# Kernel optimization log

Hardware: AMD Instinct MI355X
Metric: run time of the kernel (lower is better)

Reference implementation:

```python
import jax, jax.numpy as jnp
import numpy as np

LMAX = 4
NC = (LMAX + 1) ** 2          # 25 spherical coefficients
L0 = LMAX + 1                 # number of m=0 coefficients
SPHERE = 128
CIN1 = 2 * SPHERE             # concat(source, target) channels
HID = 64
HEADS = 8
ALPHA_C = 64
VAL_C = 16
OUT_C = 128
GRID = 2 * (LMAX + 1)         # S2 grid resolution
N_NODES = 2500
N_EDGES = 25000
MAX_ELEM = 90
EDGE_IN = 128 + 2 * 64        # distance basis + src/tgt atom embeddings
M_SIZES = [LMAX - m + 1 for m in range(1, LMAX + 1)]  # l-count per |m|>0
RAD_OUT = L0 * CIN1 + sum(s * CIN1 for s in M_SIZES)  # 3840

def _lm(l, m):
    return l * l + l + m
_p = [_lm(l, 0) for l in range(LMAX + 1)]
for m in range(1, LMAX + 1):
    _p += [_lm(l, -m) for l in range(m, LMAX + 1)]
    _p += [_lm(l, m) for l in range(m, LMAX + 1)]
PERM = np.asarray(_p)             # l-primary -> m-primary
INV_PERM = np.argsort(PERM)       # m-primary -> l-primary
EXPAND = np.concatenate([np.full(2 * l + 1, l) for l in range(LMAX + 1)])

def _layernorm(x, g, b, eps=1e-5):
    mu = jnp.mean(x, axis=-1, keepdims=True)
    var = jnp.mean((x - mu) ** 2, axis=-1, keepdims=True)
    return (x - mu) * jax.lax.rsqrt(var + eps) * g + b

def _so2_conv(xm, fc0_w, fc0_b, wms, cin, mout, extra, rad):
    # xm: [E, NC, cin] in m-primary layout. Per-order SO(2) 'complex' conv.
    E = xm.shape[0]
    x0 = xm[:, :L0].reshape(E, L0 * cin)
    off_rad = L0 * cin
    if rad is not None:
        x0 = x0 * rad[:, :off_rad]
    x0 = x0 @ fc0_w + fc0_b
    x0_extra = None
    if extra:
        x0_extra = x0[:, :extra]
        x0 = x0[:, extra:]
    outs = [x0.reshape(E, L0, mout)]
    off = L0
    for i, sz in enumerate(M_SIZES):
        xb = xm[:, off:off + 2 * sz].reshape(E, 2, sz * cin)
        if rad is not None:
            xb = xb * rad[:, off_rad:off_rad + sz * cin][:, None, :]
            off_rad += sz * cin
        y = xb @ wms[i]                         # [E, 2, 2*mout*sz]
        half = y.shape[-1] // 2
        yr, yi = y[..., :half], y[..., half:]
        o = jnp.stack([yr[:, 0] - yi[:, 1], yr[:, 1] + yi[:, 0]], axis=1)
        outs.append(o.reshape(E, 2 * sz, mout))
        off += 2 * sz
    return jnp.concatenate(outs, axis=1), x0_extra

def _segment_softmax(logits, seg, num_segments):
    mx = jax.ops.segment_max(logits, seg, num_segments=num_segments)
    ex = jnp.exp(logits - mx[seg])
    s = jax.ops.segment_sum(ex, seg, num_segments=num_segments)
    return ex / (s[seg] + 1e-16)

def setup_inputs():
    key = jax.random.key(0)
    ks = iter(jax.random.split(key, 64))
    def nrm(shape, scale=1.0):
        return jax.random.normal(next(ks), shape, dtype=jnp.float32) * scale
    def lin(i, o):
        return nrm((i, o), i ** -0.5)
    inp = {}
    inp['x'] = nrm((N_NODES, NC, SPHERE))
    inp['edge_distance'] = nrm((N_EDGES, 128))
    inp['src_table'] = jax.random.uniform(next(ks), (MAX_ELEM, 64), jnp.float32, -0.001, 0.001)
    inp['tgt_table'] = jax.random.uniform(next(ks), (MAX_ELEM, 64), jnp.float32, -0.001, 0.001)
    inp['rad_w1'] = lin(EDGE_IN, 64); inp['rad_b1'] = jnp.zeros((64,), jnp.float32)
    inp['rad_ln1_g'] = jnp.ones((64,), jnp.float32); inp['rad_ln1_b'] = jnp.zeros((64,), jnp.float32)
    inp['rad_w2'] = lin(64, 64); inp['rad_b2'] = jnp.zeros((64,), jnp.float32)
    inp['rad_ln2_g'] = jnp.ones((64,), jnp.float32); inp['rad_ln2_b'] = jnp.zeros((64,), jnp.float32)
    inp['rad_w3'] = lin(64, RAD_OUT); inp['rad_b3'] = jnp.zeros((RAD_OUT,), jnp.float32)
    inp['wigner'] = nrm((N_EDGES, NC, NC), NC ** -0.5)
    extra1 = HEADS * ALPHA_C + HID
    inp['c1_fc0_w'] = lin(L0 * CIN1, L0 * HID + extra1)
    inp['c1_fc0_b'] = jnp.zeros((L0 * HID + extra1,), jnp.float32)
    for i, sz in enumerate(M_SIZES):
        inp['c1_wm%d' % (i + 1)] = lin(sz * CIN1, 2 * HID * sz)
    inp['to_grid'] = nrm((GRID, GRID, NC), NC ** -0.5)
    inp['from_grid'] = nrm((GRID, GRID, NC), float(GRID * GRID) ** -0.5)
    inp['alpha_ln_g'] = jnp.ones((ALPHA_C,), jnp.float32)
    inp['alpha_ln_b'] = jnp.zeros((ALPHA_C,), jnp.float32)
    std = ALPHA_C ** -0.5
    inp['alpha_dot'] = jax.random.uniform(next(ks), (HEADS, ALPHA_C), jnp.float32, -std, std)
    vout = HEADS * VAL_C
    inp['c2_fc0_w'] = lin(L0 * HID, L0 * vout)
    inp['c2_fc0_b'] = jnp.zeros((L0 * vout,), jnp.float32)
    for i, sz in enumerate(M_SIZES):
        inp['c2_wm%d' % (i + 1)] = lin(sz * HID, 2 * vout * sz)
    inp['proj_w'] = nrm((L0, OUT_C, vout), vout ** -0.5)
    inp['proj_b'] = jnp.zeros((OUT_C,), jnp.float32)
    inp['atomic_numbers'] = jax.random.randint(next(ks), (N_NODES,), 0, MAX_ELEM)
    inp['edge_index'] = jax.random.randint(next(ks), (2, N_EDGES), 0, N_NODES)
    return inp

def reference(x, edge_distance, src_table, tgt_table,
              rad_w1, rad_b1, rad_ln1_g, rad_ln1_b, rad_w2, rad_b2, rad_ln2_g, rad_ln2_b, rad_w3, rad_b3,
              wigner, c1_fc0_w, c1_fc0_b, c1_wm1, c1_wm2, c1_wm3, c1_wm4,
              to_grid, from_grid, alpha_ln_g, alpha_ln_b, alpha_dot,
              c2_fc0_w, c2_fc0_b, c2_wm1, c2_wm2, c2_wm3, c2_wm4, proj_w, proj_b,
              atomic_numbers, edge_index):
    E = edge_index.shape[1]
    N = x.shape[0]
    src, tgt = edge_index[0], edge_index[1]
    # invariant edge scalars: distance basis + source/target atom embeddings
    x_edge = jnp.concatenate([edge_distance, src_table[atomic_numbers[src]], tgt_table[atomic_numbers[tgt]]], axis=1)
    # gather node embeddings to edges, rotate into edge frame (Wigner-D)
    msg = jnp.concatenate([x[src], x[tgt]], axis=2)          # [E, NC, 2*SPHERE]
    msg = jnp.einsum('eml,elc->emc', wigner, msg)
    msg = msg[:, PERM]                                        # m-primary layout
    # radial MLP producing per-(m,l,channel) edge weights
    h = jax.nn.silu(_layernorm(x_edge @ rad_w1 + rad_b1, rad_ln1_g, rad_ln1_b))
    h = jax.nn.silu(_layernorm(h @ rad_w2 + rad_b2, rad_ln2_g, rad_ln2_b))
    rad = h @ rad_w3 + rad_b3                                 # [E, RAD_OUT]
    extra1 = HEADS * ALPHA_C + HID
    msg, x0_extra = _so2_conv(msg, c1_fc0_w, c1_fc0_b, (c1_wm1, c1_wm2, c1_wm3, c1_wm4), CIN1, HID, extra1, rad)
    x0_alpha = x0_extra[:, :HEADS * ALPHA_C]
    x0_gate = x0_extra[:, HEADS * ALPHA_C:]
    # separable S2 activation: scalar SiLU on l=0, grid SiLU on l>0
    msg_l = msg[:, INV_PERM]
    grid = jax.nn.silu(jnp.einsum('bai,eic->ebac', to_grid, msg_l))
    s2 = jnp.einsum('bai,ebac->eic', from_grid, grid)
    msg_l = jnp.concatenate([jax.nn.silu(x0_gate)[:, None, :], s2[:, 1:]], axis=1)
    # second SO(2) conv (internal weights, no radial)
    msg_m = msg_l[:, PERM]
    msg_m, _ = _so2_conv(msg_m, c2_fc0_w, c2_fc0_b, (c2_wm1, c2_wm2, c2_wm3, c2_wm4), HID, HEADS * VAL_C, None, None)
    msg_l = msg_m[:, INV_PERM]
    # attention logits (LayerNorm + SmoothLeakyReLU(0.2) + dot)
    a = _layernorm(x0_alpha.reshape(E, HEADS, ALPHA_C), alpha_ln_g, alpha_ln_b)
    a = 0.6 * a + 0.4 * a * (2.0 * jax.nn.sigmoid(a) - 1.0)
    logits = jnp.einsum('ehk,hk->eh', a, alpha_dot)
    # rotate messages back to global frame (wigner_inv = wigner^T)
    msg_l = jnp.einsum('eml,emc->elc', wigner, msg_l)
    alpha = _segment_softmax(logits, tgt, N)                  # [E, HEADS]
    v = msg_l.reshape(E, NC, HEADS, VAL_C) * alpha[:, None, :, None]
    node = jax.ops.segment_sum(v.reshape(E, NC, HEADS * VAL_C), tgt, num_segments=N)
    # SO3_LinearV2 projection: per-degree linear, bias only on l=0
    out = jnp.einsum('nmi,moi->nmo', node, proj_w[EXPAND])
    out = out.at[:, 0, :].add(proj_b)
    return out
```

## Files before the change

### kernel.cpp

```cpp
#include <hip/hip_runtime.h>
#include <cstddef>

typedef unsigned short u16;
typedef __attribute__((ext_vector_type(8))) short short8;
typedef __attribute__((ext_vector_type(4))) float float4v;

__constant__ int c_PERM[25] = {0,2,6,12,20, 1,5,11,19, 3,7,13,21, 4,10,18, 8,14,22, 9,17, 15,23, 16,24};
__constant__ int c_ROFF[25] = {0,256,512,768,1024, 1280,1536,1792,2048, 1280,1536,1792,2048,
                               2304,2560,2816, 2304,2560,2816, 3072,3328, 3072,3328, 3584,3584};
__constant__ int c_EXPAND[25] = {0,1,1,1,2,2,2,2,2,3,3,3,3,3,3,3,4,4,4,4,4,4,4,4,4};

static constexpr int PERM_CE[25] = {0,2,6,12,20, 1,5,11,19, 3,7,13,21, 4,10,18, 8,14,22, 9,17, 15,23, 16,24};
static constexpr int INV_CE[25]  = {0,5,1,9,13, 6,2,10,16,19, 14,7,3,11,17, 21,23,20,15,8, 4,12,18,22,24};

__device__ __forceinline__ float wsum64(float v){
#pragma unroll
  for(int m=32;m>0;m>>=1) v += __shfl_xor(v, m, 64);
  return v;
}
__device__ __forceinline__ float siluf(float x){ return x/(1.f+expf(-x)); }

__device__ __forceinline__ void bsplit(float v, u16 &h, u16 &l){
  unsigned u = __float_as_uint(v);
  unsigned hb = (u + 0x7FFFu + ((u>>16)&1u)) >> 16;
  h = (u16)hb;
  float r = v - __uint_as_float(hb<<16);
  unsigned u2 = __float_as_uint(r);
  l = (u16)((u2 + 0x7FFFu + ((u2>>16)&1u)) >> 16);
}

__global__ __launch_bounds__(256) void wtrans_kernel(const float* __restrict__ W, u16* __restrict__ Wh, u16* __restrict__ Wl, int K, int C2){
  int idx = blockIdx.x*256 + threadIdx.x;
  int K2 = 2*K;
  if(idx >= C2*K2) return;
  int n = idx / K2, k2 = idx % K2;
  int half = C2>>1;
  float v;
  if(k2 < K) v = W[k2*C2 + n];
  else { int k = k2-K; v = (n<half) ? -W[k*C2 + half + n] : W[k*C2 + n - half]; }
  u16 h,l; bsplit(v,h,l);
  Wh[idx]=h; Wl[idx]=l;
}

__global__ __launch_bounds__(256) void fctrans_kernel(const float* __restrict__ W, u16* __restrict__ Wh, u16* __restrict__ Wl, int K, int N){
  int idx = blockIdx.x*256 + threadIdx.x;
  if(idx >= N*K) return;
  int n = idx / K, k = idx % K;
  u16 h,l; bsplit(W[(size_t)k*N + n],h,l);
  Wh[idx]=h; Wl[idx]=l;
}

__global__ __launch_bounds__(256) void ptrans_kernel(const float* __restrict__ pw, float* __restrict__ pwt){
  int idx = blockIdx.x*256+threadIdx.x;
  if(idx >= 5*16384) return;
  int l = idx>>14, r = idx & 16383, i = r>>7, o = r&127;
  pwt[idx] = pw[(l<<14) + (o<<7) + i];
}

__global__ __launch_bounds__(256) void hist_kernel(const int* __restrict__ tgt_all, int* __restrict__ cnt, int E, int C, int NN){
  int idx = blockIdx.x*256+threadIdx.x;
  if(idx>=E) return;
  atomicAdd(&cnt[(idx/C)*NN + tgt_all[idx]], 1);
}
__global__ __launch_bounds__(256) void scan_kernel(const int* __restrict__ cnt, int* __restrict__ basearr, int* __restrict__ cur, int NN, int C){
  int ch = blockIdx.x;
  __shared__ int sh[256];
  __shared__ int carry;
  if(threadIdx.x==0) carry = ch*C;
  __syncthreads();
  for(int t0=0; t0<NN; t0+=256){
    int i = t0 + threadIdx.x;
    int v = (i<NN)? cnt[ch*NN+i] : 0;
    sh[threadIdx.x]=v; __syncthreads();
    for(int off=1; off<256; off<<=1){
      int add = (threadIdx.x>=off)? sh[threadIdx.x-off]:0; __syncthreads();
      sh[threadIdx.x]+=add; __syncthreads();
    }
    int excl = carry + sh[threadIdx.x]-v;
    if(i<NN){ basearr[ch*NN+i]=excl; cur[ch*NN+i]=excl; }
    __syncthreads();
    if(threadIdx.x==255) carry += sh[255];
    __syncthreads();
  }
}
__global__ __launch_bounds__(256) void scatter_kernel(const int* __restrict__ tgt_all, int* __restrict__ cur, int* __restrict__ order, int E, int C, int NN){
  int idx = blockIdx.x*256+threadIdx.x;
  if(idx>=E) return;
  int ch = idx / C;
  int pos = atomicAdd(&cur[ch*NN + tgt_all[idx]], 1);
  order[pos] = idx;
}

__global__ __launch_bounds__(64) void radial_kernel(
    const float* __restrict__ ed, const float* __restrict__ st, const float* __restrict__ tt,
    const float* __restrict__ w1, const float* __restrict__ b1, const float* __restrict__ g1, const float* __restrict__ bb1,
    const float* __restrict__ w2, const float* __restrict__ b2, const float* __restrict__ g2, const float* __restrict__ bb2,
    const int* __restrict__ an, const int* __restrict__ src, const int* __restrict__ tgt,
    u16* __restrict__ h2h, u16* __restrict__ h2l){
  int e = blockIdx.x; int lane = threadIdx.x;
  __shared__ float xe[256];
  __shared__ float h1s[64];
  int s = src[e], t = tgt[e];
  xe[lane]      = ed[(size_t)e*128 + lane];
  xe[64+lane]   = ed[(size_t)e*128 + 64 + lane];
  int as = an[s], at = an[t];
  xe[128+lane]  = st[as*64 + lane];
  xe[192+lane]  = tt[at*64 + lane];
  __syncthreads();
  float acc = b1[lane];
  for(int k=0;k<256;k++) acc += xe[k]*w1[k*64+lane];
  float mu = wsum64(acc)*(1.f/64.f);
  float d = acc - mu;
  float var = wsum64(d*d)*(1.f/64.f);
  float nrm = d*rsqrtf(var+1e-5f)*g1[lane]+bb1[lane];
  h1s[lane] = siluf(nrm);
  __syncthreads();
  float acc2 = b2[lane];
  for(int k=0;k<64;k++) acc2 += h1s[k]*w2[k*64+lane];
  mu = wsum64(acc2)*(1.f/64.f);
  d = acc2-mu;
  var = wsum64(d*d)*(1.f/64.f);
  nrm = d*rsqrtf(var+1e-5f)*g2[lane]+bb2[lane];
  u16 h,l; bsplit(siluf(nrm),h,l);
  h2h[(size_t)e*64+lane]=h; h2l[(size_t)e*64+lane]=l;
}

struct GrpArgs {
  const u16* Ah[6]; const u16* Al[6];
  const u16* Bh[6]; const u16* Bl[6];
  const float* bias[6]; float* C1[6]; float* C2[6];
  int lda[6]; int K[6]; int ldc1[6]; int ldc2[6]; int split[6];
  int xoff[7]; int ng; int M;
};

__global__ __launch_bounds__(256) void mgemm_kernel(GrpArgs a){
  __shared__ __align__(16) u16 Ash[128*40];
  __shared__ __align__(16) u16 Asl[128*40];
  __shared__ __align__(16) u16 Bsh[128*40];
  __shared__ __align__(16) u16 Bsl[128*40];
  int bx = blockIdx.x;
  int g = 0;
  while(g+1 < a.ng && bx >= a.xoff[g+1]) g++;
  int nx = bx - a.xoff[g];
  int n0 = nx*128, m0 = blockIdx.y*128;
  const int M = a.M, K = a.K[g], lda = a.lda[g];
  const u16* __restrict__ Ah = a.Ah[g]; const u16* __restrict__ Al = a.Al[g];
  const u16* __restrict__ Bh = a.Bh[g]; const u16* __restrict__ Bl = a.Bl[g];
  int t = threadIdx.x;
  int r0 = t>>2, k80 = (t&3)*8;
  int r1 = r0 + 64;
  int ar0 = m0 + r0; if(ar0 >= M) ar0 = M-1;
  int ar1 = m0 + r1; if(ar1 >= M) ar1 = M-1;
  const u16* Ap0h = Ah + (size_t)ar0*lda + k80;
  const u16* Ap1h = Ah + (size_t)ar1*lda + k80;
  const u16* Ap0l = Al + (size_t)ar0*lda + k80;
  const u16* Ap1l = Al + (size_t)ar1*lda + k80;
  const u16* Bp0h = Bh + (size_t)(n0+r0)*K + k80;
  const u16* Bp1h = Bh + (size_t)(n0+r1)*K + k80;
  const u16* Bp0l = Bl + (size_t)(n0+r0)*K + k80;
  const u16* Bp1l = Bl + (size_t)(n0+r1)*K + k80;
  int sA = r0*40 + k80;
  int sB = r1*40 + k80;

  int wave = t>>6, lane = t&63;
  int wr = wave>>1, wc = wave&1;
  int ml = lane&15, q = lane>>4;
  int aoff = (wr*64 + ml)*40 + q*8;
  int boff = (wc*64 + ml)*40 + q*8;

  float4v acc[4][4];
#pragma unroll
  for(int i=0;i<4;i++)
#pragma unroll
    for(int j=0;j<4;j++) acc[i][j] = 0.f;

  short8 cva[4], cvb[4];
  cva[0] = *(const short8*)(Ap0h); cva[1] = *(const short8*)(Ap1h);
  cva[2] = *(const short8*)(Ap0l); cva[3] = *(const short8*)(Ap1l);
  cvb[0] = *(const short8*)(Bp0h); cvb[1] = *(const short8*)(Bp1h);
  cvb[2] = *(const short8*)(Bp0l); cvb[3] = *(const short8*)(Bp1l);

  for(int k0=0; k0<K; k0+=32){
    __syncthreads();
    *(short8*)(Ash + sA) = cva[0];
    *(short8*)(Ash + sB) = cva[1];
    *(short8*)(Asl + sA) = cva[2];
    *(short8*)(Asl + sB) = cva[3];
    *(short8*)(Bsh + sA) = cvb[0];
    *(short8*)(Bsh + sB) = cvb[1];
    *(short8*)(Bsl + sA) = cvb[2];
    *(short8*)(Bsl + sB) = cvb[3];
    __syncthreads();
    short8 nva[4], nvb[4];
    bool more = (k0+32 < K);
    if(more){
      int kn = k0+32;
      nva[0] = *(const short8*)(Ap0h + kn); nva[1] = *(const short8*)(Ap1h + kn);
      nva[2] = *(const short8*)(Ap0l + kn); nva[3] = *(const short8*)(Ap1l + kn);
      nvb[0] = *(const short8*)(Bp0h + kn); nvb[1] = *(const short8*)(Bp1h + kn);
      nvb[2] = *(const short8*)(Bp0l + kn); nvb[3] = *(const short8*)(Bp1l + kn);
    }
    short8 afh[4], afl[4];
#pragma unroll
    for(int i=0;i<4;i++){
      afh[i] = *(const short8*)(Ash + aoff + i*640);
      afl[i] = *(const short8*)(Asl + aoff + i*640);
    }
#pragma unroll
    for(int j=0;j<4;j++){
      short8 bfh = *(const short8*)(Bsh + boff + j*640);
      short8 bfl = *(const short8*)(Bsl + boff + j*640);
#pragma unroll
      for(int i=0;i<4;i++){
        acc[i][j] = __builtin_amdgcn_mfma_f32_16x16x32_bf16(afh[i], bfh, acc[i][j], 0,0,0);
        acc[i][j] = __builtin_amdgcn_mfma_f32_16x16x32_bf16(afh[i], bfl, acc[i][j], 0,0,0);
        acc[i][j] = __builtin_amdgcn_mfma_f32_16x16x32_bf16(afl[i], bfh, acc[i][j], 0,0,0);
      }
    }
    if(more){
#pragma unroll
      for(int i=0;i<4;i++){ cva[i]=nva[i]; cvb[i]=nvb[i]; }
    }
  }
  const float* bias = a.bias[g];
  int split = a.split[g];
  float* C1 = a.C1[g]; float* C2 = a.C2[g];
  int ldc1 = a.ldc1[g], ldc2 = a.ldc2[g];
#pragma unroll
  for(int i=0;i<4;i++){
    int rowb = m0 + wr*64 + i*16 + q*4;
#pragma unroll
    for(int r=0;r<4;r++){
      int row = rowb + r;
      if(row < M){
#pragma unroll
        for(int j=0;j<4;j++){
          int col = n0 + wc*64 + j*16 + ml;
          float v = acc[i][j][r];
          if(bias) v += bias[col];
          if(col < split) C1[(size_t)row*ldc1 + col] = v;
          else            C2[(size_t)row*ldc2 + (col-split)] = v;
        }
      }
    }
  }
}

__global__ __launch_bounds__(256) void wigner1_kernel(
    const float* __restrict__ x, const float* __restrict__ wigner,
    const int* __restrict__ src, const int* __restrict__ tgt,
    const float* __restrict__ rad, u16* __restrict__ msg1h, u16* __restrict__ msg1l){
  int e = blockIdx.x; int t = threadIdx.x;
  __shared__ float wig[625];
  __shared__ float4 cat4[1600];
  int s = src[e], tg = tgt[e];
  for(int i=t;i<625;i+=256) wig[i] = wigner[(size_t)e*625 + i];
  const float4* xs = (const float4*)(x + (size_t)s*3200);
  const float4* xt = (const float4*)(x + (size_t)tg*3200);
  for(int idx=t; idx<1600; idx+=256){
    int l = idx>>6, slot = idx&63;
    cat4[idx] = (slot<32) ? xs[l*32 + slot] : xt[l*32 + (slot-32)];
  }
  __syncthreads();
  int wave = t>>6, lane = t&63;
  for(int p=wave; p<25; p+=4){
    int pl = c_PERM[p];
    float4 acc = {0.f,0.f,0.f,0.f};
#pragma unroll
    for(int l=0;l<25;l++){
      float w = wig[pl*25 + l];
      float4 c = cat4[l*64 + lane];
      acc.x += w*c.x; acc.y += w*c.y; acc.z += w*c.z; acc.w += w*c.w;
    }
    float4 rd = *(const float4*)(rad + (size_t)e*3840 + c_ROFF[p] + lane*4);
    acc.x*=rd.x; acc.y*=rd.y; acc.z*=rd.z; acc.w*=rd.w;
    u16 h0,h1,h2,h3,l0,l1,l2,l3;
    bsplit(acc.x,h0,l0); bsplit(acc.y,h1,l1); bsplit(acc.z,h2,l2); bsplit(acc.w,h3,l3);
    size_t base = (size_t)e*6400 + p*256 + lane*4;
    *(uint2*)(msg1h + base) = make_uint2((unsigned)h0 | ((unsigned)h1<<16), (unsigned)h2 | ((unsigned)h3<<16));
    *(uint2*)(msg1l + base) = make_uint2((unsigned)l0 | ((unsigned)l1<<16), (unsigned)l2 | ((unsigned)l3<<16));
  }
}

__global__ __launch_bounds__(64) void grid_kernel(
    const float* __restrict__ msg2, const float* __restrict__ x0e,
    const float* __restrict__ tg, const float* __restrict__ fg,
    u16* __restrict__ m2h, u16* __restrict__ m2l){
  int e = blockIdx.x; int lane = threadIdx.x;
  float r[25];
#pragma unroll
  for(int i=0;i<25;i++) r[i] = msg2[((size_t)e*25 + INV_CE[i])*64 + lane];
  float s2[25];
#pragma unroll
  for(int i=0;i<25;i++) s2[i]=0.f;
  for(int g=0; g<100; g++){
    float tv=0.f;
#pragma unroll
    for(int i=0;i<25;i++) tv += tg[g*25+i]*r[i];
    tv = siluf(tv);
#pragma unroll
    for(int i=0;i<25;i++) s2[i] += fg[g*25+i]*tv;
  }
  float gate = siluf(x0e[(size_t)e*576 + 512 + lane]);
#pragma unroll
  for(int p=0;p<25;p++){
    int lp = PERM_CE[p];
    float v = (lp==0) ? gate : s2[lp];
    u16 h,l; bsplit(v,h,l);
    size_t idx = ((size_t)e*25+p)*64 + lane;
    m2h[idx]=h; m2l[idx]=l;
  }
}

__global__ __launch_bounds__(64) void alpha_kernel(
    const float* __restrict__ x0e, const float* __restrict__ g, const float* __restrict__ b,
    const float* __restrict__ adot, const int* __restrict__ tgt,
    float* __restrict__ exb, float* __restrict__ ssum){
  int e = blockIdx.x; int lane = threadIdx.x;
  int t = tgt[e];
  float gg = g[lane], bb = b[lane];
  for(int h=0;h<8;h++){
    float v = x0e[(size_t)e*576 + h*64 + lane];
    float mu = wsum64(v)*(1.f/64.f);
    float d = v-mu;
    float var = wsum64(d*d)*(1.f/64.f);
    float a = d*rsqrtf(var+1e-5f)*gg+bb;
    float sig = 1.f/(1.f+expf(-a));
    float a2 = 0.6f*a + 0.4f*a*(2.f*sig-1.f);
    float p = a2*adot[h*64+lane];
    float lg = wsum64(p);
    if(lane==0){
      float ex = expf(lg);
      exb[e*8+h]=ex;
      atomicAdd(&ssum[t*8+h], ex);
    }
  }
}

__global__ __launch_bounds__(256) void agg_kernel(
    const float* __restrict__ wigner_all, const float* __restrict__ msg3,
    const float* __restrict__ exb, const int* __restrict__ order,
    const int* __restrict__ basearr, const int* __restrict__ cnt,
    float* __restrict__ node, int e0){
  int n = blockIdx.x; int t = threadIdx.x;
  int lg = t>>5;
  int c4 = t&31;
  __shared__ float wig2[625];
  __shared__ float m3s[3200];
  float4v acc[4];
#pragma unroll
  for(int k=0;k<4;k++) acc[k] = 0.f;
  float* nb = node + (size_t)n*3200;
#pragma unroll
  for(int k=0;k<4;k++){ int l = lg + 8*k; if(l<25) acc[k] = *(const float4v*)(nb + l*128 + c4*4); }
  int nE = cnt[n], b0 = basearr[n];
  for(int j=0;j<nE;j++){
    int e = order[b0+j];
    int el = e - e0;
    __syncthreads();
    for(int i=t;i<625;i+=256){ int q=i/25, l=i%25; wig2[i] = wigner_all[((size_t)e*25 + c_PERM[q])*25 + l]; }
    for(int i=t;i<800;i+=256) ((float4*)m3s)[i] = ((const float4*)(msg3 + (size_t)el*3200))[i];
    __syncthreads();
    float ex = exb[el*8 + (c4>>2)];
    float4v tmp[4];
#pragma unroll
    for(int k=0;k<4;k++) tmp[k] = 0.f;
    for(int q=0;q<25;q++){
      float4v m = *(const float4v*)(m3s + q*128 + c4*4);
#pragma unroll
      for(int k=0;k<4;k++){
        int l = lg + 8*k;
        float w = (l<25) ? wig2[q*25 + l] : 0.f;
        tmp[k] += w*m;
      }
    }
#pragma unroll
    for(int k=0;k<4;k++) acc[k] += ex*tmp[k];
  }
#pragma unroll
  for(int k=0;k<4;k++){ int l = lg + 8*k; if(l<25) *(float4v*)(nb + l*128 + c4*4) = acc[k]; }
}

__global__ __launch_bounds__(256) void proj_kernel(
    const float* __restrict__ node, const float* __restrict__ ssum,
    const float* __restrict__ pwt, const float* __restrict__ proj_b,
    float* __restrict__ out, int NN){
  int n0 = blockIdx.x*2; int t = threadIdx.x;
  __shared__ float nd[2][3200];
  __shared__ float inv[2][8];
  if(t<16){
    int j=t>>3, h=t&7;
    int n=n0+j; if(n>=NN) n=NN-1;
    inv[j][h] = 1.f/(ssum[n*8+h] + 1e-16f);
  }
  __syncthreads();
  int n1 = (n0+1 < NN) ? (n0+1) : (NN-1);
  for(int i=t;i<3200;i+=256){
    int h = (i&127)>>4;
    nd[0][i] = node[(size_t)n0*3200 + i] * inv[0][h];
    nd[1][i] = node[(size_t)n1*3200 + i] * inv[1][h];
  }
  __syncthreads();
  int o = t&127, half = t>>7;
  for(int p=half;p<25;p+=2){
    int l = c_EXPAND[p];
    const float* w = pwt + l*16384;
    float a0=0.f, a1=0.f;
    for(int i=0;i<128;i++){
      float wv = w[i*128+o];
      a0 += nd[0][p*128+i]*wv;
      a1 += nd[1][p*128+i]*wv;
    }
    float bs = (p==0)? proj_b[o] : 0.f;
    out[((size_t)n0*25+p)*128 + o] = a0 + bs;
    if(n0+1 < NN) out[((size_t)(n0+1)*25+p)*128 + o] = a1 + bs;
  }
}

extern "C" void kernel_launch(void* const* d_in, const int* in_sizes, int n_in,
                              void* d_out, int out_size, void* d_ws, size_t ws_size,
                              hipStream_t stream) {
  const float* x           = (const float*)d_in[0];
  const float* edge_dist   = (const float*)d_in[1];
  const float* src_table   = (const float*)d_in[2];
  const float* tgt_table   = (const float*)d_in[3];
  const float* rad_w1      = (const float*)d_in[4];
  const float* rad_b1      = (const float*)d_in[5];
  const float* rad_ln1_g   = (const float*)d_in[6];
  const float* rad_ln1_b   = (const float*)d_in[7];
  const float* rad_w2      = (const float*)d_in[8];
  const float* rad_b2      = (const float*)d_in[9];
  const float* rad_ln2_g   = (const float*)d_in[10];
  const float* rad_ln2_b   = (const float*)d_in[11];
  const float* rad_w3      = (const float*)d_in[12];
  const float* rad_b3      = (const float*)d_in[13];
  const float* wigner      = (const float*)d_in[14];
  const float* c1_fc0_w    = (const float*)d_in[15];
  const float* c1_fc0_b    = (const float*)d_in[16];
  const float* c1_wm[4]    = {(const float*)d_in[17],(const float*)d_in[18],(const float*)d_in[19],(const float*)d_in[20]};
  const float* to_grid     = (const float*)d_in[21];
  const float* from_grid   = (const float*)d_in[22];
  const float* alpha_ln_g  = (const float*)d_in[23];
  const float* alpha_ln_b  = (const float*)d_in[24];
  const float* alpha_dot   = (const float*)d_in[25];
  const float* c2_fc0_w    = (const float*)d_in[26];
  const float* c2_fc0_b    = (const float*)d_in[27];
  const float* c2_wm[4]    = {(const float*)d_in[28],(const float*)d_in[29],(const float*)d_in[30],(const float*)d_in[31]};
  const float* proj_w      = (const float*)d_in[32];
  const float* proj_b      = (const float*)d_in[33];
  const int*   atomic_nums = (const int*)d_in[34];
  const int*   edge_index  = (const int*)d_in[35];
  float* out = (float*)d_out;
  (void)n_in; (void)out_size;

  const int E  = in_sizes[35]/2;
  const int NN = in_sizes[34];

  const int K1[4] = {1024, 768, 512, 256}, C1c[4] = {512, 384, 256, 128};
  const int K2[4] = {256, 192, 128, 64},  C2c[4] = {1024, 768, 512, 256};
  const size_t W3T = 3840*64;
  const size_t FC1 = 896*1280;
  const size_t W1S[4] = {512*2048, 384*1536, 256*1024, 128*512};
  const size_t FC2 = 640*320;
  const size_t W2S[4] = {1024*512, 768*384, 512*256, 256*128};
  size_t wush = 2*(W3T + FC1 + W1S[0]+W1S[1]+W1S[2]+W1S[3] + FC2 + W2S[0]+W2S[1]+W2S[2]+W2S[3]);
  const size_t persist = (size_t)NN*8 + (size_t)NN*3200 + wush/2 + 81920 + 4096;
  const size_t wfl = ws_size / sizeof(float);
  const int copts[10] = {25000, 12500, 6250, 5000, 3125, 2500, 1250, 625, 250, 125};
  int C = 125;
  for(int i=0;i<10;i++){
    size_t nchI = (size_t)((E + copts[i]-1)/copts[i]);
    size_t need = (size_t)copts[i]*(6400+3840+576+8) + persist + 3*nchI*NN + E;
    if(need <= wfl){ C = copts[i]; break; }
  }
  const int nch = (E + C - 1)/C;

  float* ws = (float*)d_ws;
  u16* msg1h = (u16*)ws;
  u16* msg1l = msg1h + (size_t)C*6400;
  u16* m2h   = (u16*)ws;
  u16* m2l   = m2h + (size_t)C*1600;
  float* msg3 = ws + (size_t)C*1600;
  float* rad  = ws + (size_t)C*6400;
  float* msg2 = rad;
  float* x0e  = rad + (size_t)C*3840;
  u16* h2h = (u16*)x0e;
  u16* h2l = h2h + (size_t)C*64;
  float* exb  = x0e + (size_t)C*576;
  float* ssum = exb + (size_t)C*8;
  float* node = ssum + (size_t)NN*8;
  u16* wb = (u16*)(node + (size_t)NN*3200);
  u16 *w3h = wb, *w3l = w3h + W3T;
  u16 *f1h = w3l + W3T, *f1l = f1h + FC1;
  u16 *w1h[4], *w1l[4];
  u16* p = f1l + FC1;
  for(int i=0;i<4;i++){ w1h[i]=p; w1l[i]=p+W1S[i]; p += 2*W1S[i]; }
  u16 *f2h = p, *f2l = f2h + FC2; p = f2l + FC2;
  u16 *w2h[4], *w2l[4];
  for(int i=0;i<4;i++){ w2h[i]=p; w2l[i]=p+W2S[i]; p += 2*W2S[i]; }
  float* pwt = (float*)p;
  int* cntb  = (int*)(pwt + 81920);
  int* baseb = cntb + (size_t)nch*NN;
  int* curb  = baseb + (size_t)nch*NN;
  int* order = curb + (size_t)nch*NN;

  hipMemsetAsync(node, 0, (size_t)NN*3200*sizeof(float), stream);
  hipMemsetAsync(ssum, 0, (size_t)NN*8*sizeof(float), stream);
  hipMemsetAsync(cntb, 0, (size_t)nch*NN*sizeof(int), stream);

  const int* tgt_all = edge_index + E;
  hist_kernel<<<(E+255)/256, 256, 0, stream>>>(tgt_all, cntb, E, C, NN);
  scan_kernel<<<nch, 256, 0, stream>>>(cntb, baseb, curb, NN, C);
  scatter_kernel<<<(E+255)/256, 256, 0, stream>>>(tgt_all, curb, order, E, C, NN);

  fctrans_kernel<<<((int)W3T+255)/256, 256, 0, stream>>>(rad_w3, w3h, w3l, 64, 3840);
  fctrans_kernel<<<((int)FC1+255)/256, 256, 0, stream>>>(c1_fc0_w, f1h, f1l, 1280, 896);
  fctrans_kernel<<<((int)FC2+255)/256, 256, 0, stream>>>(c2_fc0_w, f2h, f2l, 320, 640);
  for(int i=0;i<4;i++)
    wtrans_kernel<<<((int)W1S[i]*2+255)/256, 256, 0, stream>>>(c1_wm[i], w1h[i], w1l[i], K1[i], C1c[i]);
  for(int i=0;i<4;i++)
    wtrans_kernel<<<((int)W2S[i]*2+255)/256, 256, 0, stream>>>(c2_wm[i], w2h[i], w2l[i], K2[i], C2c[i]);
  ptrans_kernel<<<320, 256, 0, stream>>>(proj_w, pwt);

  const int OFF1[4] = {5,13,19,23};
  for(int ch=0; ch<nch; ch++){
    int e0 = ch*C;
    int ce = (E - e0 < C) ? (E - e0) : C;
    const int* srcp = edge_index + e0;
    const int* tgtp = edge_index + E + e0;
    const float* wigp = wigner + (size_t)e0*625;
    int mt = (ce+127)/128;

    radial_kernel<<<ce, 64, 0, stream>>>(edge_dist + (size_t)e0*128, src_table, tgt_table,
        rad_w1, rad_b1, rad_ln1_g, rad_ln1_b, rad_w2, rad_b2, rad_ln2_g, rad_ln2_b,
        atomic_nums, srcp, tgtp, h2h, h2l);

    {
      GrpArgs ga = {};
      ga.ng = 1; ga.M = ce;
      ga.Ah[0]=h2h; ga.Al[0]=h2l; ga.Bh[0]=w3h; ga.Bl[0]=w3l;
      ga.bias[0]=rad_b3; ga.C1[0]=rad; ga.C2[0]=nullptr;
      ga.lda[0]=64; ga.K[0]=64; ga.ldc1[0]=3840; ga.ldc2[0]=0; ga.split[0]=3840;
      ga.xoff[0]=0; ga.xoff[1]=30;
      mgemm_kernel<<<dim3(30, mt), 256, 0, stream>>>(ga);
    }

    wigner1_kernel<<<ce, 256, 0, stream>>>(x, wigp, srcp, tgtp, rad, msg1h, msg1l);

    {
      GrpArgs ga = {};
      ga.ng = 5; ga.M = ce;
      ga.Ah[0]=msg1h; ga.Al[0]=msg1l; ga.Bh[0]=f1h; ga.Bl[0]=f1l;
      ga.bias[0]=c1_fc0_b; ga.C1[0]=x0e; ga.C2[0]=msg2;
      ga.lda[0]=6400; ga.K[0]=1280; ga.ldc1[0]=576; ga.ldc2[0]=1600; ga.split[0]=576;
      int xo = 7;
      ga.xoff[0]=0; ga.xoff[1]=7;
      for(int i=0;i<4;i++){
        int gidx = i+1;
        ga.Ah[gidx]=msg1h + (size_t)OFF1[i]*256; ga.Al[gidx]=msg1l + (size_t)OFF1[i]*256;
        ga.Bh[gidx]=w1h[i]; ga.Bl[gidx]=w1l[i];
        ga.bias[gidx]=nullptr; ga.C1[gidx]=msg2 + OFF1[i]*64; ga.C2[gidx]=nullptr;
        ga.lda[gidx]=6400; ga.K[gidx]=2*K1[i]; ga.ldc1[gidx]=1600; ga.ldc2[gidx]=0; ga.split[gidx]=C1c[i];
        xo += C1c[i]/128;
        ga.xoff[gidx+1]=xo;
      }
      mgemm_kernel<<<dim3(xo, mt), 256, 0, stream>>>(ga);
    }

    grid_kernel<<<ce, 64, 0, stream>>>(msg2, x0e, to_grid, from_grid, m2h, m2l);
    alpha_kernel<<<ce, 64, 0, stream>>>(x0e, alpha_ln_g, alpha_ln_b, alpha_dot, tgtp, exb, ssum);

    {
      GrpArgs ga = {};
      ga.ng = 5; ga.M = ce;
      ga.Ah[0]=m2h; ga.Al[0]=m2l; ga.Bh[0]=f2h; ga.Bl[0]=f2l;
      ga.bias[0]=c2_fc0_b; ga.C1[0]=msg3; ga.C2[0]=nullptr;
      ga.lda[0]=1600; ga.K[0]=320; ga.ldc1[0]=3200; ga.ldc2[0]=0; ga.split[0]=640;
      int xo = 5;
      ga.xoff[0]=0; ga.xoff[1]=5;
      for(int i=0;i<4;i++){
        int gidx = i+1;
        ga.Ah[gidx]=m2h + (size_t)OFF1[i]*64; ga.Al[gidx]=m2l + (size_t)OFF1[i]*64;
        ga.Bh[gidx]=w2h[i]; ga.Bl[gidx]=w2l[i];
        ga.bias[gidx]=nullptr; ga.C1[gidx]=msg3 + OFF1[i]*128; ga.C2[gidx]=nullptr;
        ga.lda[gidx]=1600; ga.K[gidx]=2*K2[i]; ga.ldc1[gidx]=3200; ga.ldc2[gidx]=0; ga.split[gidx]=C2c[i];
        xo += C2c[i]/128;
        ga.xoff[gidx+1]=xo;
      }
      mgemm_kernel<<<dim3(xo, mt), 256, 0, stream>>>(ga);
    }

    agg_kernel<<<NN, 256, 0, stream>>>(wigner, msg3, exb, order,
        baseb + (size_t)ch*NN, cntb + (size_t)ch*NN, node, e0);
  }

  proj_kernel<<<(NN+1)/2, 256, 0, stream>>>(node, ssum, pwt, proj_b, out, NN);
}
```

Baseline: 3.661 ms.

## Double-buffer GEMM LDS with XOR swizzle, XCD-aware tile mapping, halve radial buffer

The grouped bf16x3 GEMM gets double-buffered shared-memory tiles, so there is one barrier per k-step instead of two. The padded 40-stride layout is replaced by an XOR-swizzled 32-stride layout to avoid bank conflicts. Blocks are remapped so each XCD works on a contiguous range of N tiles, which should improve L2 reuse on the multi-die GPU. The radial/wigner stage now runs in two halves per chunk so the radial buffer only needs half the size, which frees workspace and can allow larger chunks, at the cost of extra launches.

```diff
diff --git a/kernel.cpp b/kernel.cpp
--- a/kernel.cpp
+++ b/kernel.cpp
@@ -130,49 +130,58 @@
   const u16* Bh[6]; const u16* Bl[6];
   const float* bias[6]; float* C1[6]; float* C2[6];
   int lda[6]; int K[6]; int ldc1[6]; int ldc2[6]; int split[6];
-  int xoff[7]; int ng; int M;
+  int xoff[7]; int ng; int M; int gx; int gy;
 };
 
 __global__ __launch_bounds__(256) void mgemm_kernel(GrpArgs a){
-  __shared__ __align__(16) u16 Ash[128*40];
-  __shared__ __align__(16) u16 Asl[128*40];
-  __shared__ __align__(16) u16 Bsh[128*40];
-  __shared__ __align__(16) u16 Bsl[128*40];
-  int bx = blockIdx.x;
+  __shared__ __align__(16) u16 Ash[2][4096];
+  __shared__ __align__(16) u16 Asl[2][4096];
+  __shared__ __align__(16) u16 Bsh[2][4096];
+  __shared__ __align__(16) u16 Bsl[2][4096];
+
+  int b = blockIdx.x;
+  int xcd = b & 7, i = b >> 3;
+  int pbase = a.gx >> 3, prem = a.gx & 7;
+  int s = pbase + (xcd < prem ? 1 : 0);
+  if(i >= s * a.gy) return;
+  int o = xcd*pbase + (xcd < prem ? xcd : prem);
+  int xt = o + (i % s);
+  int yt = i / s;
+
   int g = 0;
-  while(g+1 < a.ng && bx >= a.xoff[g+1]) g++;
-  int nx = bx - a.xoff[g];
-  int n0 = nx*128, m0 = blockIdx.y*128;
+  while(g+1 < a.ng && xt >= a.xoff[g+1]) g++;
+  int n0 = (xt - a.xoff[g])*128, m0 = yt*128;
   const int M = a.M, K = a.K[g], lda = a.lda[g];
   const u16* __restrict__ Ah = a.Ah[g]; const u16* __restrict__ Al = a.Al[g];
   const u16* __restrict__ Bh = a.Bh[g]; const u16* __restrict__ Bl = a.Bl[g];
   int t = threadIdx.x;
-  int r0 = t>>2, k80 = (t&3)*8;
-  int r1 = r0 + 64;
+  int r0 = t>>2, kblk = t&3, k80 = kblk*8;
   int ar0 = m0 + r0; if(ar0 >= M) ar0 = M-1;
-  int ar1 = m0 + r1; if(ar1 >= M) ar1 = M-1;
+  int ar1 = m0 + r0 + 64; if(ar1 >= M) ar1 = M-1;
   const u16* Ap0h = Ah + (size_t)ar0*lda + k80;
   const u16* Ap1h = Ah + (size_t)ar1*lda + k80;
   const u16* Ap0l = Al + (size_t)ar0*lda + k80;
   const u16* Ap1l = Al + (size_t)ar1*lda + k80;
   const u16* Bp0h = Bh + (size_t)(n0+r0)*K + k80;
-  const u16* Bp1h = Bh + (size_t)(n0+r1)*K + k80;
+  const u16* Bp1h = Bh + (size_t)(n0+r0+64)*K + k80;
   const u16* Bp0l = Bl + (size_t)(n0+r0)*K + k80;
-  const u16* Bp1l = Bl + (size_t)(n0+r1)*K + k80;
-  int sA = r0*40 + k80;
-  int sB = r1*40 + k80;
+  const u16* Bp1l = Bl + (size_t)(n0+r0+64)*K + k80;
+  int pcbS = kblk ^ ((r0>>1)&3);
+  int sA = r0*32 + pcbS*8;
+  int sB = sA + 64*32;
 
   int wave = t>>6, lane = t&63;
   int wr = wave>>1, wc = wave&1;
   int ml = lane&15, q = lane>>4;
-  int aoff = (wr*64 + ml)*40 + q*8;
-  int boff = (wc*64 + ml)*40 + q*8;
+  int pcbA = q ^ ((ml>>1)&3);
+  int aoff = (wr*64 + ml)*32 + pcbA*8;
+  int boff = (wc*64 + ml)*32 + pcbA*8;
 
   float4v acc[4][4];
 #pragma unroll
-  for(int i=0;i<4;i++)
-#pragma unroll
-    for(int j=0;j<4;j++) acc[i][j] = 0.f;
+  for(int i2=0;i2<4;i2++)
+#pragma unroll
+    for(int j=0;j<4;j++) acc[i2][j] = 0.f;
 
   short8 cva[4], cvb[4];
   cva[0] = *(const short8*)(Ap0h); cva[1] = *(const short8*)(Ap1h);
@@ -180,55 +189,50 @@
   cvb[0] = *(const short8*)(Bp0h); cvb[1] = *(const short8*)(Bp1h);
   cvb[2] = *(const short8*)(Bp0l); cvb[3] = *(const short8*)(Bp1l);
 
+  int p = 0;
   for(int k0=0; k0<K; k0+=32){
+    *(short8*)(&Ash[p][sA]) = cva[0];
+    *(short8*)(&Ash[p][sB]) = cva[1];
+    *(short8*)(&Asl[p][sA]) = cva[2];
+    *(short8*)(&Asl[p][sB]) = cva[3];
+    *(short8*)(&Bsh[p][sA]) = cvb[0];
+    *(short8*)(&Bsh[p][sB]) = cvb[1];
+    *(short8*)(&Bsl[p][sA]) = cvb[2];
+    *(short8*)(&Bsl[p][sB]) = cvb[3];
+    if(k0+32 < K){
+      int kn = k0+32;
+      cva[0] = *(const short8*)(Ap0h + kn); cva[1] = *(const short8*)(Ap1h + kn);
+      cva[2] = *(const short8*)(Ap0l + kn); cva[3] = *(const short8*)(Ap1l + kn);
+      cvb[0] = *(const short8*)(Bp0h + kn); cvb[1] = *(const short8*)(Bp1h + kn);
+      cvb[2] = *(const short8*)(Bp0l + kn); cvb[3] = *(const short8*)(Bp1l + kn);
+    }
     __syncthreads();
-    *(short8*)(Ash + sA) = cva[0];
-    *(short8*)(Ash + sB) = cva[1];
-    *(short8*)(Asl + sA) = cva[2];
-    *(short8*)(Asl + sB) = cva[3];
-    *(short8*)(Bsh + sA) = cvb[0];
-    *(short8*)(Bsh + sB) = cvb[1];
-    *(short8*)(Bsl + sA) = cvb[2];
-    *(short8*)(Bsl + sB) = cvb[3];
-    __syncthreads();
-    short8 nva[4], nvb[4];
-    bool more = (k0+32 < K);
-    if(more){
-      int kn = k0+32;
-      nva[0] = *(const short8*)(Ap0h + kn); nva[1] = *(const short8*)(Ap1h + kn);
-      nva[2] = *(const short8*)(Ap0l + kn); nva[3] = *(const short8*)(Ap1l + kn);
-      nvb[0] = *(const short8*)(Bp0h + kn); nvb[1] = *(const short8*)(Bp1h + kn);
-      nvb[2] = *(const short8*)(Bp0l + kn); nvb[3] = *(const short8*)(Bp1l + kn);
-    }
     short8 afh[4], afl[4];
 #pragma unroll
-    for(int i=0;i<4;i++){
-      afh[i] = *(const short8*)(Ash + aoff + i*640);
-      afl[i] = *(const short8*)(Asl + aoff + i*640);
+    for(int i2=0;i2<4;i2++){
+      afh[i2] = *(const short8*)(&Ash[p][aoff + i2*512]);
+      afl[i2] = *(const short8*)(&Asl[p][aoff + i2*512]);
     }
 #pragma unroll
     for(int j=0;j<4;j++){
-      short8 bfh = *(const short8*)(Bsh + boff + j*640);
-      short8 bfl = *(const short8*)(Bsl + boff + j*640);
-#pragma unroll
-      for(int i=0;i<4;i++){
-        acc[i][j] = __builtin_amdgcn_mfma_f32_16x16x32_bf16(afh[i], bfh, acc[i][j], 0,0,0);
-        acc[i][j] = __builtin_amdgcn_mfma_f32_16x16x32_bf16(afh[i], bfl, acc[i][j], 0,0,0);
-        acc[i][j] = __builtin_amdgcn_mfma_f32_16x16x32_bf16(afl[i], bfh, acc[i][j], 0,0,0);
+      short8 bfh = *(const short8*)(&Bsh[p][boff + j*512]);
+      short8 bfl = *(const short8*)(&Bsl[p][boff + j*512]);
+#pragma unroll
+      for(int i2=0;i2<4;i2++){
+        acc[i2][j] = __builtin_amdgcn_mfma_f32_16x16x32_bf16(afh[i2], bfh, acc[i2][j], 0,0,0);
+        acc[i2][j] = __builtin_amdgcn_mfma_f32_16x16x32_bf16(afh[i2], bfl, acc[i2][j], 0,0,0);
+        acc[i2][j] = __builtin_amdgcn_mfma_f32_16x16x32_bf16(afl[i2], bfh, acc[i2][j], 0,0,0);
       }
     }
-    if(more){
-#pragma unroll
-      for(int i=0;i<4;i++){ cva[i]=nva[i]; cvb[i]=nvb[i]; }
-    }
+    p ^= 1;
   }
   const float* bias = a.bias[g];
   int split = a.split[g];
   float* C1 = a.C1[g]; float* C2 = a.C2[g];
   int ldc1 = a.ldc1[g], ldc2 = a.ldc2[g];
 #pragma unroll
-  for(int i=0;i<4;i++){
-    int rowb = m0 + wr*64 + i*16 + q*4;
+  for(int i2=0;i2<4;i2++){
+    int rowb = m0 + wr*64 + i2*16 + q*4;
 #pragma unroll
     for(int r=0;r<4;r++){
       int row = rowb + r;
@@ -236,7 +240,7 @@
 #pragma unroll
         for(int j=0;j<4;j++){
           int col = n0 + wc*64 + j*16 + ml;
-          float v = acc[i][j][r];
+          float v = acc[i2][j][r];
           if(bias) v += bias[col];
           if(col < split) C1[(size_t)row*ldc1 + col] = v;
           else            C2[(size_t)row*ldc2 + (col-split)] = v;
@@ -464,16 +468,18 @@
   const size_t FC2 = 640*320;
   const size_t W2S[4] = {1024*512, 768*384, 512*256, 256*128};
   size_t wush = 2*(W3T + FC1 + W1S[0]+W1S[1]+W1S[2]+W1S[3] + FC2 + W2S[0]+W2S[1]+W2S[2]+W2S[3]);
-  const size_t persist = (size_t)NN*8 + (size_t)NN*3200 + wush/2 + 81920 + 4096;
+  const size_t persist = (size_t)NN*8 + (size_t)NN*3200 + wush/2 + 81920 + 8192;
   const size_t wfl = ws_size / sizeof(float);
   const int copts[10] = {25000, 12500, 6250, 5000, 3125, 2500, 1250, 625, 250, 125};
   int C = 125;
   for(int i=0;i<10;i++){
     size_t nchI = (size_t)((E + copts[i]-1)/copts[i]);
-    size_t need = (size_t)copts[i]*(6400+3840+576+8) + persist + 3*nchI*NN + E;
+    size_t hc = (size_t)(copts[i]+1)/2;
+    size_t need = (size_t)copts[i]*(6400+576+8) + hc*3840 + persist + 3*nchI*NN + E;
     if(need <= wfl){ C = copts[i]; break; }
   }
   const int nch = (E + C - 1)/C;
+  const size_t halfC = (size_t)(C+1)/2;
 
   float* ws = (float*)d_ws;
   u16* msg1h = (u16*)ws;
@@ -483,9 +489,9 @@
   float* msg3 = ws + (size_t)C*1600;
   float* rad  = ws + (size_t)C*6400;
   float* msg2 = rad;
-  float* x0e  = rad + (size_t)C*3840;
+  float* x0e  = rad + halfC*3840;
   u16* h2h = (u16*)x0e;
-  u16* h2l = h2h + (size_t)C*64;
+  u16* h2l = h2h + halfC*64;
   float* exb  = x0e + (size_t)C*576;
   float* ssum = exb + (size_t)C*8;
   float* node = ssum + (size_t)NN*8;
@@ -522,6 +528,13 @@
     wtrans_kernel<<<((int)W2S[i]*2+255)/256, 256, 0, stream>>>(c2_wm[i], w2h[i], w2l[i], K2[i], C2c[i]);
   ptrans_kernel<<<320, 256, 0, stream>>>(proj_w, pwt);
 
+  auto launchM = [&](GrpArgs &ga, int gx, int gy){
+    ga.gx = gx; ga.gy = gy;
+    int base = gx>>3, rem = gx&7;
+    int maxs = base + (rem?1:0);
+    mgemm_kernel<<<8*maxs*gy, 256, 0, stream>>>(ga);
+  };
+
   const int OFF1[4] = {5,13,19,23};
   for(int ch=0; ch<nch; ch++){
     int e0 = ch*C;
@@ -531,21 +544,26 @@
     const float* wigp = wigner + (size_t)e0*625;
     int mt = (ce+127)/128;
 
-    radial_kernel<<<ce, 64, 0, stream>>>(edge_dist + (size_t)e0*128, src_table, tgt_table,
-        rad_w1, rad_b1, rad_ln1_g, rad_ln1_b, rad_w2, rad_b2, rad_ln2_g, rad_ln2_b,
-        atomic_nums, srcp, tgtp, h2h, h2l);
-
-    {
-      GrpArgs ga = {};
-      ga.ng = 1; ga.M = ce;
-      ga.Ah[0]=h2h; ga.Al[0]=h2l; ga.Bh[0]=w3h; ga.Bl[0]=w3l;
-      ga.bias[0]=rad_b3; ga.C1[0]=rad; ga.C2[0]=nullptr;
-      ga.lda[0]=64; ga.K[0]=64; ga.ldc1[0]=3840; ga.ldc2[0]=0; ga.split[0]=3840;
-      ga.xoff[0]=0; ga.xoff[1]=30;
-      mgemm_kernel<<<dim3(30, mt), 256, 0, stream>>>(ga);
-    }
-
-    wigner1_kernel<<<ce, 256, 0, stream>>>(x, wigp, srcp, tgtp, rad, msg1h, msg1l);
+    int half1 = (ce+1)/2;
+    for(int hh=0; hh<2; hh++){
+      int h0 = hh ? half1 : 0;
+      int he = hh ? (ce - half1) : half1;
+      if(he <= 0) continue;
+      radial_kernel<<<he, 64, 0, stream>>>(edge_dist + (size_t)(e0+h0)*128, src_table, tgt_table,
+          rad_w1, rad_b1, rad_ln1_g, rad_ln1_b, rad_w2, rad_b2, rad_ln2_g, rad_ln2_b,
+          atomic_nums, srcp+h0, tgtp+h0, h2h, h2l);
+      {
+        GrpArgs ga = {};
+        ga.ng = 1; ga.M = he;
+        ga.Ah[0]=h2h; ga.Al[0]=h2l; ga.Bh[0]=w3h; ga.Bl[0]=w3l;
+        ga.bias[0]=rad_b3; ga.C1[0]=rad; ga.C2[0]=nullptr;
+        ga.lda[0]=64; ga.K[0]=64; ga.ldc1[0]=3840; ga.ldc2[0]=0; ga.split[0]=3840;
+        ga.xoff[0]=0; ga.xoff[1]=30;
+        launchM(ga, 30, (he+127)/128);
+      }
+      wigner1_kernel<<<he, 256, 0, stream>>>(x, wigp + (size_t)h0*625, srcp+h0, tgtp+h0, rad,
+          msg1h + (size_t)h0*6400, msg1l + (size_t)h0*6400);
+    }
 
     {
       GrpArgs ga = {};
@@ -564,7 +582,7 @@
         xo += C1c[i]/128;
         ga.xoff[gidx+1]=xo;
       }
-      mgemm_kernel<<<dim3(xo, mt), 256, 0, stream>>>(ga);
+      launchM(ga, xo, mt);
     }
 
     grid_kernel<<<ce, 64, 0, stream>>>(msg2, x0e, to_grid, from_grid, m2h, m2l);
@@ -587,7 +605,7 @@
         xo += C2c[i]/128;
         ga.xoff[gidx+1]=xo;
       }
-      mgemm_kernel<<<dim3(xo, mt), 256, 0, stream>>>(ga);
+      launchM(ga, xo, mt);
     }
 
     agg_kernel<<<NN, 256, 0, stream>>>(wigner, msg3, exb, order,
```

Measured after the change: 3.585 ms. 2.1% less time.
